# Kernel tuning notes

Measured on AMD Instinct MI355X. Metric: run time of the kernel, lower is better.

## Reference

```python
import jax, jax.numpy as jnp
import numpy as np

B, H, W, C = 16, 32, 32, 512
NUM_HEADS = 8
ATTN_DIM = 512
HEAD_DIM = ATTN_DIM // NUM_HEADS
EPS = 1e-5


def setup_inputs() -> dict:
    key = jax.random.key(0)
    ks = jax.random.split(key, 6)
    s_in = 1.0 / np.sqrt(C)
    s_attn = 1.0 / np.sqrt(ATTN_DIM)
    return {
        "x": jax.random.normal(ks[0], (B, H, W, C), dtype=jnp.float32),
        "gamma": jnp.ones((C,), dtype=jnp.float32),
        "beta": jnp.zeros((C,), dtype=jnp.float32),
        "wq": jax.random.normal(ks[1], (C, ATTN_DIM), dtype=jnp.float32) * s_in,
        "bq": jnp.zeros((ATTN_DIM,), dtype=jnp.float32),
        "wk": jax.random.normal(ks[2], (C, ATTN_DIM), dtype=jnp.float32) * s_in,
        "bk": jnp.zeros((ATTN_DIM,), dtype=jnp.float32),
        "wv": jax.random.normal(ks[3], (C, ATTN_DIM), dtype=jnp.float32) * s_in,
        "bv": jnp.zeros((ATTN_DIM,), dtype=jnp.float32),
        "wo": jax.random.normal(ks[4], (ATTN_DIM, C), dtype=jnp.float32) * s_attn,
        "bo": jnp.zeros((C,), dtype=jnp.float32),
    }


def reference(x, gamma, beta, wq, bq, wk, bk, wv, bv, wo, bo):
    b, h, w, c = x.shape
    t = h * w  # number of spatial tokens
    # GroupNorm with 1 group: normalize over (H, W, C) per sample
    mean = jnp.mean(x, axis=(1, 2, 3), keepdims=True)
    var = jnp.var(x, axis=(1, 2, 3), keepdims=True)
    xn = (x - mean) * jax.lax.rsqrt(var + EPS) * gamma + beta
    xn = xn.reshape(b, t, c)
    # 1x1-conv q/k/v == dense over channel dim; split into heads
    q = (xn @ wq + bq).reshape(b, t, NUM_HEADS, HEAD_DIM)
    k = (xn @ wk + bk).reshape(b, t, NUM_HEADS, HEAD_DIM)
    v = (xn @ wv + bv).reshape(b, t, NUM_HEADS, HEAD_DIM)
    scale = 1.0 / jnp.sqrt(jnp.asarray(HEAD_DIM, dtype=x.dtype))
    scores = jnp.einsum('bqhd,bkhd->bhqk', q, k) * scale
    probs = jax.nn.softmax(scores, axis=-1)
    attn = jnp.einsum('bhqk,bkhd->bqhd', probs, v).reshape(b, t, ATTN_DIM)
    out = attn @ wo + bo
    # Multiplex([None, branch]): residual add, then Reshape([-1, model_dim])
    return x.reshape(b, t, c) + out
```

## Files before the change

kernel.cpp:

```cpp
#include <hip/hip_runtime.h>
#include <hip/hip_bf16.h>

typedef __attribute__((ext_vector_type(8))) short short8;
typedef __attribute__((ext_vector_type(4))) short short4v;
typedef __attribute__((ext_vector_type(4))) float f32x4;

#define B_ 16
#define T_ 1024
#define C_ 512
#define NH 8
#define HD 64

__device__ __forceinline__ short f2bf(float f) {
  union { float f; unsigned u; } v;
  v.f = f;
  unsigned r = v.u + 0x7fffu + ((v.u >> 16) & 1u);
  return (short)(r >> 16);
}

__device__ __forceinline__ short2 pack_bf2(float a, float b) {
  __hip_bfloat162 t = __float22bfloat162_rn(make_float2(a, b));
  short2 r;
  __builtin_memcpy(&r, &t, 4);
  return r;
}

__device__ __forceinline__ void gload_lds16(const short* g, short* l) {
  __builtin_amdgcn_global_load_lds(
      (const __attribute__((address_space(1))) void*)g,
      (__attribute__((address_space(3))) void*)l, 16, 0, 0);
}

__global__ __launch_bounds__(256) void stats1_kernel(const float* __restrict__ x,
                                                     float2* __restrict__ partials) {
  int chunk = blockIdx.x;
  int b = blockIdx.y;
  int tid = threadIdx.x;
  const float4* xb = (const float4*)(x + (size_t)b * 524288 + (size_t)chunk * 8192);
  float s = 0.f, s2 = 0.f;
#pragma unroll
  for (int i = 0; i < 8; i++) {
    float4 v = xb[tid + i * 256];
    s  += v.x + v.y + v.z + v.w;
    s2 += v.x * v.x + v.y * v.y + v.z * v.z + v.w * v.w;
  }
  __shared__ float ls[256], ls2[256];
  ls[tid] = s; ls2[tid] = s2;
  __syncthreads();
  for (int o = 128; o > 0; o >>= 1) {
    if (tid < o) { ls[tid] += ls[tid + o]; ls2[tid] += ls2[tid + o]; }
    __syncthreads();
  }
  if (tid == 0) partials[b * 64 + chunk] = make_float2(ls[0], ls2[0]);
}

__global__ __launch_bounds__(64) void stats2_kernel(const float2* __restrict__ partials,
                                                    float* __restrict__ stats) {
  int b = blockIdx.x;
  float2 p = partials[b * 64 + threadIdx.x];
  float s = p.x, s2 = p.y;
#pragma unroll
  for (int off = 1; off < 64; off <<= 1) {
    s  += __shfl_xor(s,  off, 64);
    s2 += __shfl_xor(s2, off, 64);
  }
  if (threadIdx.x == 0) {
    float mean = s * (1.f / 524288.f);
    float var  = s2 * (1.f / 524288.f) - mean * mean;
    stats[b * 2]     = mean;
    stats[b * 2 + 1] = rsqrtf(var + 1e-5f);
  }
}

__global__ __launch_bounds__(256) void norm_kernel(const float* __restrict__ x,
                                                   const float* __restrict__ gamma,
                                                   const float* __restrict__ beta,
                                                   const float* __restrict__ stats,
                                                   short* __restrict__ xn) {
  size_t i4 = (size_t)blockIdx.x * 256 + threadIdx.x;
  float4 v = ((const float4*)x)[i4];
  size_t i = i4 * 4;
  int b = (int)(i >> 19);
  int c = (int)(i & 511);
  float mean = stats[b * 2], rstd = stats[b * 2 + 1];
  short4v o;
  o[0] = f2bf((v.x - mean) * rstd * gamma[c + 0] + beta[c + 0]);
  o[1] = f2bf((v.y - mean) * rstd * gamma[c + 1] + beta[c + 1]);
  o[2] = f2bf((v.z - mean) * rstd * gamma[c + 2] + beta[c + 2]);
  o[3] = f2bf((v.w - mean) * rstd * gamma[c + 3] + beta[c + 3]);
  ((short4v*)xn)[i4] = o;
}

__global__ __launch_bounds__(256) void transpose_w_all(const float* __restrict__ wq,
                                                       const float* __restrict__ wk,
                                                       const float* __restrict__ wv,
                                                       const float* __restrict__ wo,
                                                       short* __restrict__ wqkvT,
                                                       short* __restrict__ woT) {
  int o = blockIdx.x * 256 + threadIdx.x;
  int sel = o >> 18;
  int oo = o & 262143;
  int k = oo >> 9, n = oo & 511;
  const float* w = (sel == 0) ? wq : (sel == 1) ? wk : (sel == 2) ? wv : wo;
  float val = w[oo];
  if (sel < 3) wqkvT[((size_t)(sel * 512 + n)) * 512 + k] = f2bf(val);
  else         woT[(size_t)n * 512 + k] = f2bf(val);
}

__global__ __launch_bounds__(256) void gemm_qkv(const short* __restrict__ A,
                                                const short* __restrict__ Bt,
                                                const float* __restrict__ bq,
                                                const float* __restrict__ bk,
                                                const float* __restrict__ bv,
                                                short* __restrict__ C) {
  __shared__ __align__(16) short As[128 * 32];
  __shared__ __align__(16) short Bs[128 * 32];
  int tid = threadIdx.x;
  int w = tid >> 6, lane = tid & 63;
  int quad = lane >> 4, l16 = lane & 15;
  int mw = (w >> 1) * 64, nw = (w & 1) * 64;
  int seg = (blockIdx.x * 128) >> 9;
  const float* bias = (seg == 0) ? bq : (seg == 1) ? bk : bv;
  float smul = (seg == 0) ? 0.125f : 1.0f;
  const short* Atile = A + (size_t)(blockIdx.y * 128) * 512;
  const short* Btile = Bt + (size_t)(blockIdx.x * 128) * 512;
  int srow = (w << 4) + (lane >> 2);
  int scol = (lane & 3) * 8;
  f32x4 acc[4][4] = {};
  for (int k0 = 0; k0 < 512; k0 += 32) {
    __syncthreads();
    gload_lds16(&Atile[(size_t)srow * 512 + k0 + scol],        &As[w * 512]);
    gload_lds16(&Atile[(size_t)(srow + 64) * 512 + k0 + scol], &As[2048 + w * 512]);
    gload_lds16(&Btile[(size_t)srow * 512 + k0 + scol],        &Bs[w * 512]);
    gload_lds16(&Btile[(size_t)(srow + 64) * 512 + k0 + scol], &Bs[2048 + w * 512]);
    __syncthreads();
    short8 af[4], bf[4];
#pragma unroll
    for (int i = 0; i < 4; i++) af[i] = *(const short8*)(&As[(mw + i * 16 + l16) * 32 + quad * 8]);
#pragma unroll
    for (int i = 0; i < 4; i++) bf[i] = *(const short8*)(&Bs[(nw + i * 16 + l16) * 32 + quad * 8]);
#pragma unroll
    for (int mi = 0; mi < 4; mi++)
#pragma unroll
      for (int ni = 0; ni < 4; ni++)
        acc[mi][ni] = __builtin_amdgcn_mfma_f32_16x16x32_bf16(af[mi], bf[ni], acc[mi][ni], 0, 0, 0);
  }
  int m0 = blockIdx.y * 128 + mw;
  int n0 = blockIdx.x * 128 + nw;
#pragma unroll
  for (int mi = 0; mi < 4; mi++)
#pragma unroll
    for (int ni = 0; ni < 4; ni++) {
      int col = n0 + ni * 16 + l16;
      float bval = bias[col & 511];
#pragma unroll
      for (int r = 0; r < 4; r++) {
        int row = m0 + mi * 16 + quad * 4 + r;
        C[(size_t)row * 1536 + col] = f2bf((acc[mi][ni][r] + bval) * smul);
      }
    }
}

__global__ __launch_bounds__(256) void gemm_out(const short* __restrict__ A,
                                                const short* __restrict__ Bt,
                                                const float* __restrict__ bias,
                                                const float* __restrict__ xres,
                                                float* __restrict__ out) {
  __shared__ __align__(16) short As[128 * 32];
  __shared__ __align__(16) short Bs[128 * 32];
  int tid = threadIdx.x;
  int w = tid >> 6, lane = tid & 63;
  int quad = lane >> 4, l16 = lane & 15;
  int mw = (w >> 1) * 64, nw = (w & 1) * 64;
  const short* Atile = A + (size_t)(blockIdx.y * 128) * 512;
  const short* Btile = Bt + (size_t)(blockIdx.x * 128) * 512;
  int srow = (w << 4) + (lane >> 2);
  int scol = (lane & 3) * 8;
  f32x4 acc[4][4] = {};
  for (int k0 = 0; k0 < 512; k0 += 32) {
    __syncthreads();
    gload_lds16(&Atile[(size_t)srow * 512 + k0 + scol],        &As[w * 512]);
    gload_lds16(&Atile[(size_t)(srow + 64) * 512 + k0 + scol], &As[2048 + w * 512]);
    gload_lds16(&Btile[(size_t)srow * 512 + k0 + scol],        &Bs[w * 512]);
    gload_lds16(&Btile[(size_t)(srow + 64) * 512 + k0 + scol], &Bs[2048 + w * 512]);
    __syncthreads();
    short8 af[4], bf[4];
#pragma unroll
    for (int i = 0; i < 4; i++) af[i] = *(const short8*)(&As[(mw + i * 16 + l16) * 32 + quad * 8]);
#pragma unroll
    for (int i = 0; i < 4; i++) bf[i] = *(const short8*)(&Bs[(nw + i * 16 + l16) * 32 + quad * 8]);
#pragma unroll
    for (int mi = 0; mi < 4; mi++)
#pragma unroll
      for (int ni = 0; ni < 4; ni++)
        acc[mi][ni] = __builtin_amdgcn_mfma_f32_16x16x32_bf16(af[mi], bf[ni], acc[mi][ni], 0, 0, 0);
  }
  int m0 = blockIdx.y * 128 + mw;
  int n0 = blockIdx.x * 128 + nw;
#pragma unroll
  for (int mi = 0; mi < 4; mi++)
#pragma unroll
    for (int ni = 0; ni < 4; ni++) {
      int col = n0 + ni * 16 + l16;
      float bval = bias[col];
#pragma unroll
      for (int r = 0; r < 4; r++) {
        int row = m0 + mi * 16 + quad * 4 + r;
        out[(size_t)row * 512 + col] = acc[mi][ni][r] + bval + xres[(size_t)row * 512 + col];
      }
    }
}

__global__ __launch_bounds__(256) void vtrans_kernel(const short* __restrict__ qkv,
                                                     short* __restrict__ vT) {
  int chunk = blockIdx.x;
  int h  = blockIdx.y;
  int b  = blockIdx.z;
  int tid = threadIdx.x;
  __shared__ short TB[128 * 72];
  const short* src = qkv + ((size_t)b * T_ + chunk * 128) * 1536 + 1024 + (size_t)h * 64;
#pragma unroll
  for (int i = 0; i < 4; i++) {
    int idx = tid + i * 256;
    int t = idx >> 3, c = idx & 7;
    *(short8*)(&TB[t * 72 + c * 8]) = *(const short8*)(src + (size_t)t * 1536 + c * 8);
  }
  __syncthreads();
  short* dst = vT + ((size_t)(b * 8 + h) * 64) * 1024 + chunk * 128;
#pragma unroll
  for (int i = 0; i < 4; i++) {
    int idx = tid + i * 256;
    int d = idx >> 4, sc = idx & 15;
    int w2 = sc >> 2, q2 = sc & 3;
    short8 o;
#pragma unroll
    for (int sg = 0; sg < 8; sg++) {
      int half = sg >> 2, r = sg & 3;
      o[sg] = TB[(half * 64 + w2 * 16 + q2 * 4 + r) * 72 + d];
    }
    *(short8*)(dst + (size_t)d * 1024 + sc * 8) = o;
  }
}

__global__ __launch_bounds__(256) void attn_kernel(const short* __restrict__ Q,
                                                   const short* __restrict__ Kmat,
                                                   const short* __restrict__ vTg,
                                                   short* __restrict__ O) {
  int tid = threadIdx.x;
  int w = tid >> 6, lane = tid & 63;
  int quad = lane >> 4, l16 = lane & 15;
  int bh = blockIdx.x;
  int qt = blockIdx.y;
  int b = bh >> 3, h = bh & 7;
  size_t base  = ((size_t)b * T_) * 1536 + (size_t)h * 64;
  size_t vbase = ((size_t)bh * 64) * 1024;
  size_t obase = ((size_t)b * T_) * 512 + (size_t)h * 64;
  int qrow0 = qt * 64;

  __shared__ __align__(16) char smem[32768 + 1024];
  short* KT = (short*)smem;
  short* VT = (short*)(smem + 16384);
  float* Lbuf = (float*)smem;
  float* denomL = (float*)(smem + 32768);

  short8 qf0[4], qf1[4];
#pragma unroll
  for (int g = 0; g < 4; g++) {
    const short* qp = Q + base + (size_t)(qrow0 + g * 16 + l16) * 1536 + quad * 8;
    qf0[g] = *(const short8*)qp;
    qf1[g] = *(const short8*)(qp + 32);
  }

  const short* ksrc[4];
  const short* vsrc[4];
#pragma unroll
  for (int n = 0; n < 4; n++) {
    int bk = w * 256 + n * 64 + lane;
    int key = bk >> 3, jc = bk & 7;
    int dcol = jc ^ (key & 7);
    ksrc[n] = Kmat + base + (size_t)key * 1536 + dcol * 8;
    int d = bk >> 4, j = bk & 15;
    int kc = j ^ (d & 15);
    vsrc[n] = vTg + vbase + (size_t)d * 1024 + kc * 8;
  }

  int l7 = l16 & 7;
  int kA0 = ((w * 16 + l16) * 8 + (quad ^ l7)) * 8;
  int kA1 = ((w * 16 + l16) * 8 + ((quad + 4) ^ l7)) * 8;
  int kB0 = kA0 + 4096;
  int kB1 = kA1 + 4096;
  int vOff = (l16 * 16 + ((w * 4 + quad) ^ l16)) * 8;

  f32x4 oacc[4][4] = {};
  float lsum[4] = {0.f, 0.f, 0.f, 0.f};

  for (int kk0 = 0; kk0 < T_; kk0 += 128) {
    __syncthreads();
#pragma unroll
    for (int n = 0; n < 4; n++)
      gload_lds16(ksrc[n] + (size_t)kk0 * 1536, KT + (w * 256 + n * 64) * 8);
#pragma unroll
    for (int n = 0; n < 4; n++)
      gload_lds16(vsrc[n] + kk0, VT + (w * 256 + n * 64) * 8);
    __syncthreads();

    short8 kfa0 = *(const short8*)(KT + kA0);
    short8 kfa1 = *(const short8*)(KT + kA1);
    short8 kfb0 = *(const short8*)(KT + kB0);
    short8 kfb1 = *(const short8*)(KT + kB1);
    short8 vfr[4];
#pragma unroll
    for (int f = 0; f < 4; f++) vfr[f] = *(const short8*)(VT + vOff + f * 2048);

#pragma unroll
    for (int g = 0; g < 4; g++) {
      f32x4 za = {}, zb = {};
      za = __builtin_amdgcn_mfma_f32_16x16x32_bf16(kfa0, qf0[g], za, 0, 0, 0);
      za = __builtin_amdgcn_mfma_f32_16x16x32_bf16(kfa1, qf1[g], za, 0, 0, 0);
      zb = __builtin_amdgcn_mfma_f32_16x16x32_bf16(kfb0, qf0[g], zb, 0, 0, 0);
      zb = __builtin_amdgcn_mfma_f32_16x16x32_bf16(kfb1, qf1[g], zb, 0, 0, 0);
      float pa0 = __expf(za[0]), pa1 = __expf(za[1]);
      float pa2 = __expf(za[2]), pa3 = __expf(za[3]);
      float pb0 = __expf(zb[0]), pb1 = __expf(zb[1]);
      float pb2 = __expf(zb[2]), pb3 = __expf(zb[3]);
      lsum[g] += (pa0 + pa1) + (pa2 + pa3) + (pb0 + pb1) + (pb2 + pb3);
      short2 a01 = pack_bf2(pa0, pa1), a23 = pack_bf2(pa2, pa3);
      short2 b01 = pack_bf2(pb0, pb1), b23 = pack_bf2(pb2, pb3);
      short8 pf;
      pf[0] = a01.x; pf[1] = a01.y; pf[2] = a23.x; pf[3] = a23.y;
      pf[4] = b01.x; pf[5] = b01.y; pf[6] = b23.x; pf[7] = b23.y;
#pragma unroll
      for (int f = 0; f < 4; f++)
        oacc[f][g] = __builtin_amdgcn_mfma_f32_16x16x32_bf16(vfr[f], pf, oacc[f][g], 0, 0, 0);
    }
  }

#pragma unroll
  for (int g = 0; g < 4; g++) {
    lsum[g] += __shfl_xor(lsum[g], 16, 64);
    lsum[g] += __shfl_xor(lsum[g], 32, 64);
  }
  if (quad == 0) {
#pragma unroll
    for (int g = 0; g < 4; g++) denomL[w * 64 + g * 16 + l16] = lsum[g];
  }
  for (int ww = 0; ww < 4; ww++) {
    __syncthreads();
    if (w == ww) {
#pragma unroll
      for (int g = 0; g < 4; g++)
#pragma unroll
        for (int f = 0; f < 4; f++) {
          float* p = &Lbuf[(g * 16 + l16) * 68 + f * 16 + quad * 4];
          if (ww == 0) *(f32x4*)p = oacc[f][g];
          else         *(f32x4*)p = *(f32x4*)p + oacc[f][g];
        }
    }
  }
  __syncthreads();

  int q = tid >> 2, seg = tid & 3;
  float dn = denomL[q] + denomL[64 + q] + denomL[128 + q] + denomL[192 + q];
  float rinv = __frcp_rn(dn);
  const float* row = &Lbuf[q * 68 + seg * 16];
  short8 o0, o1;
#pragma unroll
  for (int i = 0; i < 8; i++) o0[i] = f2bf(row[i] * rinv);
#pragma unroll
  for (int i = 0; i < 8; i++) o1[i] = f2bf(row[8 + i] * rinv);
  short* op = O + obase + (size_t)(qrow0 + q) * 512 + seg * 16;
  *(short8*)op = o0;
  *(short8*)(op + 8) = o1;
}

extern "C" void kernel_launch(void* const* d_in, const int* in_sizes, int n_in,
                              void* d_out, int out_size, void* d_ws, size_t ws_size,
                              hipStream_t stream) {
  const float* x     = (const float*)d_in[0];
  const float* gamma = (const float*)d_in[1];
  const float* beta  = (const float*)d_in[2];
  const float* wq    = (const float*)d_in[3];
  const float* bq    = (const float*)d_in[4];
  const float* wk    = (const float*)d_in[5];
  const float* bk    = (const float*)d_in[6];
  const float* wv    = (const float*)d_in[7];
  const float* bv    = (const float*)d_in[8];
  const float* wo    = (const float*)d_in[9];
  const float* bo    = (const float*)d_in[10];
  float* out = (float*)d_out;

  char* ws = (char*)d_ws;
  const size_t XN_ELEMS = (size_t)B_ * T_ * C_;
  size_t off = 0;
  float* stats = (float*)(ws + off); off += 256;
  float2* partials = (float2*)(ws + off); off += 16 * 64 * sizeof(float2);
  short* xn    = (short*)(ws + off); off += XN_ELEMS * 2;
  short* wqkvT = (short*)(ws + off); off += (size_t)1536 * 512 * 2;
  short* woT   = (short*)(ws + off); off += (size_t)512 * 512 * 2;
  short* qkv   = (short*)(ws + off); off += (size_t)B_ * T_ * 1536 * 2;
  short* vTb   = (short*)(ws + off); off += XN_ELEMS * 2;
  short* ao    = (short*)(ws + off); off += XN_ELEMS * 2;

  stats1_kernel<<<dim3(64, 16), 256, 0, stream>>>(x, partials);
  stats2_kernel<<<16, 64, 0, stream>>>(partials, stats);
  norm_kernel<<<8192, 256, 0, stream>>>(x, gamma, beta, stats, xn);
  transpose_w_all<<<4096, 256, 0, stream>>>(wq, wk, wv, wo, wqkvT, woT);

  gemm_qkv<<<dim3(12, 128), 256, 0, stream>>>(xn, wqkvT, bq, bk, bv, qkv);

  vtrans_kernel<<<dim3(8, 8, 16), 256, 0, stream>>>(qkv, vTb);
  attn_kernel<<<dim3(128, 16), 256, 0, stream>>>(qkv, qkv + 512, vTb, ao);

  gemm_out<<<dim3(4, 128), 256, 0, stream>>>(ao, woT, bo, x, out);
}
```

Before: 248.4 us.

## Load attention K/V fragments directly from global memory with register prefetch

The attention kernel stops staging K and V tiles through LDS with barriers. Each wave now loads its own MFMA fragments straight from global memory and prefetches the next K tile into registers, so the loop is fully unrolled and needs no synchronisation. Separately, log2(e) is folded into the Q scale so the softmax can use the raw v_exp_f32 (exp2) instruction instead of __expf. The change lowers shared-memory use, which may raise occupancy, but it gives up cross-wave reuse of the loaded tiles and issues more uncoalesced 16-byte global loads per wave.

New measurement: 254.1 us. +2.3%, slower.

```diff
diff --git a/kernel.cpp b/kernel.cpp
--- a/kernel.cpp
+++ b/kernel.cpp
@@ -22,6 +22,12 @@
   __hip_bfloat162 t = __float22bfloat162_rn(make_float2(a, b));
   short2 r;
   __builtin_memcpy(&r, &t, 4);
+  return r;
+}
+
+__device__ __forceinline__ float fexp2(float x) {
+  float r;
+  asm("v_exp_f32 %0, %1" : "=v"(r) : "v"(x));
   return r;
 }
 
@@ -121,7 +127,7 @@
   int mw = (w >> 1) * 64, nw = (w & 1) * 64;
   int seg = (blockIdx.x * 128) >> 9;
   const float* bias = (seg == 0) ? bq : (seg == 1) ? bk : bv;
-  float smul = (seg == 0) ? 0.125f : 1.0f;
+  float smul = (seg == 0) ? 0.18033688011112042f : 1.0f;
   const short* Atile = A + (size_t)(blockIdx.y * 128) * 512;
   const short* Btile = Bt + (size_t)(blockIdx.x * 128) * 512;
   int srow = (w << 4) + (lane >> 2);
@@ -257,11 +263,9 @@
   size_t obase = ((size_t)b * T_) * 512 + (size_t)h * 64;
   int qrow0 = qt * 64;
 
-  __shared__ __align__(16) char smem[32768 + 1024];
-  short* KT = (short*)smem;
-  short* VT = (short*)(smem + 16384);
+  __shared__ __align__(16) char smem[17408 + 1024];
   float* Lbuf = (float*)smem;
-  float* denomL = (float*)(smem + 32768);
+  float* denomL = (float*)(smem + 17408);
 
   short8 qf0[4], qf1[4];
 #pragma unroll
@@ -271,59 +275,45 @@
     qf1[g] = *(const short8*)(qp + 32);
   }
 
-  const short* ksrc[4];
-  const short* vsrc[4];
-#pragma unroll
-  for (int n = 0; n < 4; n++) {
-    int bk = w * 256 + n * 64 + lane;
-    int key = bk >> 3, jc = bk & 7;
-    int dcol = jc ^ (key & 7);
-    ksrc[n] = Kmat + base + (size_t)key * 1536 + dcol * 8;
-    int d = bk >> 4, j = bk & 15;
-    int kc = j ^ (d & 15);
-    vsrc[n] = vTg + vbase + (size_t)d * 1024 + kc * 8;
-  }
-
-  int l7 = l16 & 7;
-  int kA0 = ((w * 16 + l16) * 8 + (quad ^ l7)) * 8;
-  int kA1 = ((w * 16 + l16) * 8 + ((quad + 4) ^ l7)) * 8;
-  int kB0 = kA0 + 4096;
-  int kB1 = kA1 + 4096;
-  int vOff = (l16 * 16 + ((w * 4 + quad) ^ l16)) * 8;
+  const short* kp0 = Kmat + base + (size_t)(w * 16 + l16) * 1536 + quad * 8;
+  const short* kp1 = kp0 + 64 * 1536;
+  const short* vp0 = vTg + vbase + (size_t)l16 * 1024 + (w * 4 + quad) * 8;
 
   f32x4 oacc[4][4] = {};
   float lsum[4] = {0.f, 0.f, 0.f, 0.f};
 
-  for (int kk0 = 0; kk0 < T_; kk0 += 128) {
-    __syncthreads();
-#pragma unroll
-    for (int n = 0; n < 4; n++)
-      gload_lds16(ksrc[n] + (size_t)kk0 * 1536, KT + (w * 256 + n * 64) * 8);
-#pragma unroll
-    for (int n = 0; n < 4; n++)
-      gload_lds16(vsrc[n] + kk0, VT + (w * 256 + n * 64) * 8);
-    __syncthreads();
-
-    short8 kfa0 = *(const short8*)(KT + kA0);
-    short8 kfa1 = *(const short8*)(KT + kA1);
-    short8 kfb0 = *(const short8*)(KT + kB0);
-    short8 kfb1 = *(const short8*)(KT + kB1);
+  short8 ka0 = *(const short8*)kp0;
+  short8 ka1 = *(const short8*)(kp0 + 32);
+  short8 ka2 = *(const short8*)kp1;
+  short8 ka3 = *(const short8*)(kp1 + 32);
+
+#pragma unroll
+  for (int t = 0; t < 8; t++) {
     short8 vfr[4];
 #pragma unroll
-    for (int f = 0; f < 4; f++) vfr[f] = *(const short8*)(VT + vOff + f * 2048);
-
+    for (int f = 0; f < 4; f++)
+      vfr[f] = *(const short8*)(vp0 + (size_t)f * 16384 + t * 128);
+    short8 kn0, kn1, kn2, kn3;
+    if (t < 7) {
+      const short* p0 = kp0 + (size_t)(t + 1) * 196608;
+      const short* p1 = kp1 + (size_t)(t + 1) * 196608;
+      kn0 = *(const short8*)p0;
+      kn1 = *(const short8*)(p0 + 32);
+      kn2 = *(const short8*)p1;
+      kn3 = *(const short8*)(p1 + 32);
+    }
 #pragma unroll
     for (int g = 0; g < 4; g++) {
       f32x4 za = {}, zb = {};
-      za = __builtin_amdgcn_mfma_f32_16x16x32_bf16(kfa0, qf0[g], za, 0, 0, 0);
-      za = __builtin_amdgcn_mfma_f32_16x16x32_bf16(kfa1, qf1[g], za, 0, 0, 0);
-      zb = __builtin_amdgcn_mfma_f32_16x16x32_bf16(kfb0, qf0[g], zb, 0, 0, 0);
-      zb = __builtin_amdgcn_mfma_f32_16x16x32_bf16(kfb1, qf1[g], zb, 0, 0, 0);
-      float pa0 = __expf(za[0]), pa1 = __expf(za[1]);
-      float pa2 = __expf(za[2]), pa3 = __expf(za[3]);
-      float pb0 = __expf(zb[0]), pb1 = __expf(zb[1]);
-      float pb2 = __expf(zb[2]), pb3 = __expf(zb[3]);
-      lsum[g] += (pa0 + pa1) + (pa2 + pa3) + (pb0 + pb1) + (pb2 + pb3);
+      za = __builtin_amdgcn_mfma_f32_16x16x32_bf16(ka0, qf0[g], za, 0, 0, 0);
+      za = __builtin_amdgcn_mfma_f32_16x16x32_bf16(ka1, qf1[g], za, 0, 0, 0);
+      zb = __builtin_amdgcn_mfma_f32_16x16x32_bf16(ka2, qf0[g], zb, 0, 0, 0);
+      zb = __builtin_amdgcn_mfma_f32_16x16x32_bf16(ka3, qf1[g], zb, 0, 0, 0);
+      float pa0 = fexp2(za[0]), pa1 = fexp2(za[1]);
+      float pa2 = fexp2(za[2]), pa3 = fexp2(za[3]);
+      float pb0 = fexp2(zb[0]), pb1 = fexp2(zb[1]);
+      float pb2 = fexp2(zb[2]), pb3 = fexp2(zb[3]);
+      lsum[g] += (pa0 + pa1) + (pa2 + pa3) + ((pb0 + pb1) + (pb2 + pb3));
       short2 a01 = pack_bf2(pa0, pa1), a23 = pack_bf2(pa2, pa3);
       short2 b01 = pack_bf2(pb0, pb1), b23 = pack_bf2(pb2, pb3);
       short8 pf;
@@ -333,6 +323,7 @@
       for (int f = 0; f < 4; f++)
         oacc[f][g] = __builtin_amdgcn_mfma_f32_16x16x32_bf16(vfr[f], pf, oacc[f][g], 0, 0, 0);
     }
+    if (t < 7) { ka0 = kn0; ka1 = kn1; ka2 = kn2; ka3 = kn3; }
   }
 
 #pragma unroll
```
